# Kernel tuning notes

Measured on AMD Instinct MI355X. Metric: run time of the kernel, lower is better.

The kernel has to match this reference:

```python
import jax, jax.numpy as jnp
import numpy as np

EPS = 1e-12  # F.normalize default eps (denominator = max(norm, eps))


def setup_inputs() -> dict:
    key = jax.random.key(0)
    ks = jax.random.split(key, 8)
    B, FIN, H, W = 4, 256, 64, 64
    N_MEM, SQ = 64, 16           # sqrt_fin = fin**0.5
    POS_CH = 2                    # PosEncoding concatenates one coord channel per dim
    CIN = FIN + POS_CH
    QK = N_MEM * SQ               # 1024
    # PosEncoding buffer: normalized coordinate grid in [-1, 1], shape [2, H, W]
    ys = jnp.linspace(-1.0, 1.0, H, dtype=jnp.float32)
    xs = jnp.linspace(-1.0, 1.0, W, dtype=jnp.float32)
    gy, gx = jnp.meshgrid(ys, xs, indexing='ij')
    pos = jnp.stack([gy, gx], axis=0)
    s = 0.02
    return {
        'x':    jax.random.normal(ks[0], (B, FIN, H, W), jnp.float32),
        'pos':  pos,
        'wq':   jax.random.normal(ks[1], (QK, CIN), jnp.float32) * s,
        'bq':   jnp.zeros((QK,), jnp.float32),
        'wk':   jax.random.normal(ks[2], (QK, CIN), jnp.float32) * s,
        'bk':   jnp.zeros((QK,), jnp.float32),
        'v':    jax.random.normal(ks[3], (N_MEM, FIN), jnp.float32) * s,
        'wout': jax.random.normal(ks[4], (FIN, FIN), jnp.float32) * s,
        'bout': jnp.zeros((FIN,), jnp.float32),
    }


def reference(x, pos, wq, bq, wk, bk, v, wout, bout):
    B, C, H, W = x.shape
    S = H * W
    n_mem, fin = v.shape
    sq = wq.shape[0] // n_mem
    # PosEncoding: concat coordinate channels
    posb = jnp.broadcast_to(pos[None], (B,) + pos.shape)
    xp = jnp.concatenate([x, posb], axis=1).reshape(B, C + pos.shape[0], S)
    # 1x1 conv projections (channel GEMMs)
    q = jnp.einsum('oc,bcs->bos', wq, xp) + bq[None, :, None]  # [B, n_mem*sq, S]
    k = jnp.einsum('oc,bcs->bos', wk, xp) + bk[None, :, None]
    q = q.reshape(B, n_mem, sq, S).transpose(0, 3, 1, 2)  # [B,S,m,sq]
    k = k.reshape(B, n_mem, sq, S).transpose(0, 3, 2, 1)  # [B,S,sq,m]
    # F.normalize: q over last dim (sqrt_fin), k over dim=1 (sqrt_fin)
    qn = q / jnp.maximum(jnp.linalg.norm(q, axis=-1, keepdims=True), EPS)
    kn = k / jnp.maximum(jnp.linalg.norm(k, axis=2, keepdims=True), EPS)
    # attn[b,s,m,n] = qn . kn ; dropout is identity in eval mode.
    # mean over memory slots m commutes with (attn @ v), so fuse:
    attn_mean = jnp.einsum('bsk,bskn->bsn', qn.mean(axis=2), kn)  # [B,S,n_mem]
    mem = attn_mean @ v                                            # [B,S,fin]
    mem = mem.transpose(0, 2, 1).reshape(B, fin, H, W)
    out = jnp.einsum('of,bfhw->bohw', wout, mem) + bout[None, :, None, None]
    return x + out
```

## Files before the change

kernel.cpp:

```cpp
#include <hip/hip_runtime.h>
#include <stdint.h>

#define EPSN 1e-12f

typedef float f32x16 __attribute__((ext_vector_type(16)));
typedef float f32x4 __attribute__((ext_vector_type(4)));
typedef __bf16 bf16x8 __attribute__((ext_vector_type(8)));
typedef unsigned short u16x4 __attribute__((ext_vector_type(4)));

__device__ __forceinline__ unsigned short f2bf(float f) {
  union { float f; unsigned int u; } v; v.f = f;
  unsigned int u = v.u + 0x7FFFu + ((v.u >> 16) & 1u);
  return (unsigned short)(u >> 16);
}
__device__ __forceinline__ float bf2f(unsigned short h) {
  union { float f; unsigned int u; } v; v.u = ((unsigned int)h) << 16;
  return v.f;
}

#define NKS 17
#define WQF_OFF 0
#define WKF_OFF (32 * NKS * 64 * 8)
#define WVP_OFF (2 * 32 * NKS * 64 * 8)

__global__ __launch_bounds__(256) void prep_kernel(
    const float* __restrict__ wq, const float* __restrict__ bq,
    const float* __restrict__ wk, const float* __restrict__ bk,
    const float* __restrict__ v, const float* __restrict__ wout,
    unsigned short* __restrict__ wsp) {
  int bid = blockIdx.x;
  if (bid < 512) {
    int isK = bid >= 256;
    int ob = (bid & 255) * 4;
    const float* w = isK ? wk : wq;
    const float* bb = isK ? bk : bq;
    unsigned short* dst = wsp + (isK ? WKF_OFF : WQF_OFF);
    for (int i = threadIdx.x; i < 4 * 129; i += 256) {
      int r = i / 129, q = i - r * 129;
      int o = ob + r, k = q * 2;
      float2 w2 = *(const float2*)(w + o * 258 + k);
      int g = o >> 5, col = o & 31;
      int ks = k >> 4, hi = (k >> 3) & 1, j = k & 7;
      uint32_t pk = (uint32_t)f2bf(w2.x) | ((uint32_t)f2bf(w2.y) << 16);
      *(uint32_t*)(dst + (((g * NKS + ks) * 64 + hi * 32 + col) << 3) + j) = pk;
    }
    for (int i = threadIdx.x; i < 4 * 14; i += 256) {
      int r = i / 14, kk = 258 + (i - r * 14);
      int o = ob + r;
      int g = o >> 5, col = o & 31;
      int ks = kk >> 4, hi = (kk >> 3) & 1, j = kk & 7;
      dst[(((g * NKS + ks) * 64 + hi * 32 + col) << 3) + j] =
          (kk == 258) ? f2bf(bb[o]) : (unsigned short)0;
    }
  } else {
    int idx = (bid - 512) * 256 + threadIdx.x;
    int fc = idx & 15, m = (idx >> 4) & 63, o = idx >> 10;
    const f32x4* wo = (const f32x4*)(wout + o * 256 + fc * 16);
    const f32x4* vm = (const f32x4*)(v + m * 256 + fc * 16);
    float s = 0.f;
#pragma unroll
    for (int f = 0; f < 4; ++f) {
      f32x4 a = wo[f], bvv = vm[f];
      s += a[0]*bvv[0] + a[1]*bvv[1] + a[2]*bvv[2] + a[3]*bvv[3];
    }
    s += __shfl_xor(s, 1, 64);
    s += __shfl_xor(s, 2, 64);
    s += __shfl_xor(s, 4, 64);
    s += __shfl_xor(s, 8, 64);
    if (fc == 0) wsp[WVP_OFF + o * 64 + m] = f2bf(s);
  }
}

#define PXB 64
#define KP 296
#define QS 66
#define AT 72

__global__ __launch_bounds__(1024, 4) void fused_kernel(
    const float* __restrict__ x, const float* __restrict__ pos,
    const unsigned short* __restrict__ wsp, const float* __restrict__ bout,
    float* __restrict__ out) {
  __shared__ __align__(16) unsigned short xp[PXB * KP];
  __shared__ __align__(16) float qbarL[16 * QS];
  __shared__ __align__(16) unsigned short attnM[PXB * AT];
  __shared__ float boutL[256];

  const int tid = threadIdx.x;
  const int lane = tid & 63;
  const int wid = __builtin_amdgcn_readfirstlane(tid >> 6);
  const int px = lane & 31, q2 = lane >> 5;
  const int P0 = blockIdx.x * PXB;
  const int b = P0 >> 12, s0 = P0 & 4095;

  const int wtoff = (2 * wid) * NKS * 512 + lane * 8;
  const unsigned short* wqf = wsp + WQF_OFF + wtoff;
  const unsigned short* wkf = wsp + WKF_OFF + wtoff;

  uint32_t* xp32 = (uint32_t*)xp;
  {
    const float* xrow = x + b * 256 * 4096 + s0;
    f32x4 lo[2], hi[2];
#pragma unroll
    for (int it = 0; it < 2; ++it) {
      int idx = tid + it * 1024;
      int g = idx & 15, dcol = idx >> 4;
      lo[it] = __builtin_nontemporal_load(
          (const f32x4*)(xrow + (2 * dcol) * 4096 + 4 * g));
      hi[it] = __builtin_nontemporal_load(
          (const f32x4*)(xrow + (2 * dcol + 1) * 4096 + 4 * g));
    }
#pragma unroll
    for (int it = 0; it < 2; ++it) {
      int idx = tid + it * 1024;
      int g = idx & 15, dcol = idx >> 4;
#pragma unroll
      for (int j = 0; j < 4; ++j) {
        int pp = 4 * g + j;
        xp32[pp * 148 + dcol] =
            (uint32_t)f2bf(lo[it][j]) | ((uint32_t)f2bf(hi[it][j]) << 16);
      }
    }
    if (tid < 512) {
      int pp = tid & 63, dcol = 128 + (tid >> 6);
      float t0 = 0.f, t1 = 0.f;
      if (dcol == 128) { t0 = pos[s0 + pp]; t1 = pos[4096 + s0 + pp]; }
      else if (dcol == 129) { t0 = 1.0f; }
      xp32[pp * 148 + dcol] = (uint32_t)f2bf(t0) | ((uint32_t)f2bf(t1) << 16);
    }
  }
  if (tid < 256) boutL[tid] = bout[tid];
  for (int i = tid; i < 16 * QS; i += 1024) qbarL[i] = 0.f;
  __syncthreads();

#define PHASE(WB) do {                                                    \
    const unsigned short* _p0 = (WB);                                     \
    const unsigned short* _p1 = (WB) + NKS * 512;                         \
    const unsigned short* _bp0 = &xp[px * KP + q2 * 8];                   \
    const unsigned short* _bp1 = &xp[(32 + px) * KP + q2 * 8];            \
    bf16x8 _A0c = *(const bf16x8*)_p0;                                    \
    bf16x8 _A1c = *(const bf16x8*)_p1;                                    \
    _Pragma("unroll 1")                                                   \
    for (int i = 0; i < NKS - 1; ++i) {                                   \
      bf16x8 _A0n = *(const bf16x8*)(_p0 + (i + 1) * 512);                \
      bf16x8 _A1n = *(const bf16x8*)(_p1 + (i + 1) * 512);                \
      bf16x8 _b0 = *(const bf16x8*)(_bp0 + i * 16);                       \
      bf16x8 _b1 = *(const bf16x8*)(_bp1 + i * 16);                       \
      __builtin_amdgcn_s_setprio(1);                                      \
      acc00 = __builtin_amdgcn_mfma_f32_32x32x16_bf16(_A0c, _b0, acc00, 0, 0, 0); \
      acc01 = __builtin_amdgcn_mfma_f32_32x32x16_bf16(_A0c, _b1, acc01, 0, 0, 0); \
      acc10 = __builtin_amdgcn_mfma_f32_32x32x16_bf16(_A1c, _b0, acc10, 0, 0, 0); \
      acc11 = __builtin_amdgcn_mfma_f32_32x32x16_bf16(_A1c, _b1, acc11, 0, 0, 0); \
      __builtin_amdgcn_s_setprio(0);                                      \
      _A0c = _A0n; _A1c = _A1n;                                           \
    }                                                                     \
    {                                                                     \
      bf16x8 _b0 = *(const bf16x8*)(_bp0 + (NKS - 1) * 16);               \
      bf16x8 _b1 = *(const bf16x8*)(_bp1 + (NKS - 1) * 16);               \
      acc00 = __builtin_amdgcn_mfma_f32_32x32x16_bf16(_A0c, _b0, acc00, 0, 0, 0); \
      acc01 = __builtin_amdgcn_mfma_f32_32x32x16_bf16(_A0c, _b1, acc01, 0, 0, 0); \
      acc10 = __builtin_amdgcn_mfma_f32_32x32x16_bf16(_A1c, _b0, acc10, 0, 0, 0); \
      acc11 = __builtin_amdgcn_mfma_f32_32x32x16_bf16(_A1c, _b1, acc11, 0, 0, 0); \
    }                                                                     \
  } while (0)

  f32x16 acc00 = (f32x16)0.f, acc01 = (f32x16)0.f,
         acc10 = (f32x16)0.f, acc11 = (f32x16)0.f;
  PHASE(wqf);

  {
    float qsum[2][8];
#pragma unroll
    for (int nt = 0; nt < 2; ++nt)
#pragma unroll
      for (int r = 0; r < 8; ++r) qsum[nt][r] = 0.f;
#pragma unroll
    for (int ot = 0; ot < 2; ++ot) {
#pragma unroll
      for (int nt = 0; nt < 2; ++nt) {
        const f32x16 a = ot ? (nt ? acc11 : acc10) : (nt ? acc01 : acc00);
        float s20 = 0.f, s21 = 0.f;
#pragma unroll
        for (int r = 0; r < 8; ++r) {
          s20 = fmaf(a[r], a[r], s20);
          s21 = fmaf(a[r + 8], a[r + 8], s21);
        }
        s20 += __shfl_xor(s20, 32, 64);
        s21 += __shfl_xor(s21, 32, 64);
        float i0 = 1.0f / fmaxf(sqrtf(s20), EPSN);
        float i1 = 1.0f / fmaxf(sqrtf(s21), EPSN);
#pragma unroll
        for (int r = 0; r < 8; ++r) qsum[nt][r] += a[r] * i0 + a[r + 8] * i1;
      }
    }
#pragma unroll
    for (int nt = 0; nt < 2; ++nt)
#pragma unroll
      for (int r = 0; r < 8; ++r) {
        int j = (r & 3) + ((r >> 2) << 3) + (q2 << 2);
        atomicAdd(&qbarL[j * QS + nt * 32 + px], qsum[nt][r] * (1.0f / 64.0f));
      }
  }

  acc00 = (f32x16)0.f; acc01 = (f32x16)0.f;
  acc10 = (f32x16)0.f; acc11 = (f32x16)0.f;
  PHASE(wkf);
  __syncthreads();

  {
    float qb[2][8];
#pragma unroll
    for (int nt = 0; nt < 2; ++nt)
#pragma unroll
      for (int r = 0; r < 8; ++r) {
        int j = (r & 3) + ((r >> 2) << 3) + (q2 << 2);
        qb[nt][r] = qbarL[j * QS + nt * 32 + px];
      }
#pragma unroll
    for (int ot = 0; ot < 2; ++ot) {
#pragma unroll
      for (int nt = 0; nt < 2; ++nt) {
        const f32x16 a = ot ? (nt ? acc11 : acc10) : (nt ? acc01 : acc00);
        float s20 = 0.f, s21 = 0.f, sp0 = 0.f, sp1 = 0.f;
#pragma unroll
        for (int r = 0; r < 8; ++r) {
          s20 = fmaf(a[r], a[r], s20);         sp0 = fmaf(qb[nt][r], a[r], sp0);
          s21 = fmaf(a[r + 8], a[r + 8], s21); sp1 = fmaf(qb[nt][r], a[r + 8], sp1);
        }
        s20 += __shfl_xor(s20, 32, 64);
        s21 += __shfl_xor(s21, 32, 64);
        sp0 += __shfl_xor(sp0, 32, 64);
        sp1 += __shfl_xor(sp1, 32, 64);
        if (q2 == 0) {
          int m0 = wid * 4 + ot * 2;
          attnM[(nt * 32 + px) * AT + m0]     = f2bf(sp0 / fmaxf(sqrtf(s20), EPSN));
          attnM[(nt * 32 + px) * AT + m0 + 1] = f2bf(sp1 / fmaxf(sqrtf(s21), EPSN));
        }
      }
    }
  }
  __syncthreads();

  {
    const int otile = wid >> 1, pxt = wid & 1;
    f32x16 e = (f32x16)0.f;
    const unsigned short* wv = wsp + WVP_OFF + (otile * 32 + px) * 64 + q2 * 8;
    const unsigned short* ab = &attnM[(pxt * 32 + px) * AT + q2 * 8];
#pragma unroll
    for (int ks = 0; ks < 4; ++ks) {
      bf16x8 av = *(const bf16x8*)(wv + ks * 16);
      bf16x8 bv = *(const bf16x8*)(ab + ks * 16);
      e = __builtin_amdgcn_mfma_f32_32x32x16_bf16(av, bv, e, 0, 0, 0);
    }
    const int p = pxt * 32 + px;
    const unsigned short* xl = &xp[p * KP + otile * 32 + (q2 << 2)];
#pragma unroll
    for (int rq = 0; rq < 4; ++rq) {
      u16x4 xq = *(const u16x4*)(xl + 8 * rq);
#pragma unroll
      for (int j = 0; j < 4; ++j) {
        const int r = rq * 4 + j;
        const int o = otile * 32 + j + (rq << 3) + (q2 << 2);
        const int gi = (b * 256 + o) * 4096 + s0 + p;
        __builtin_nontemporal_store(bf2f(xq[j]) + boutL[o] + e[r], &out[gi]);
      }
    }
  }
#undef PHASE
}

extern "C" void kernel_launch(void* const* d_in, const int* in_sizes, int n_in,
                              void* d_out, int out_size, void* d_ws, size_t ws_size,
                              hipStream_t stream) {
  const float* x    = (const float*)d_in[0];
  const float* pos  = (const float*)d_in[1];
  const float* wq   = (const float*)d_in[2];
  const float* bq   = (const float*)d_in[3];
  const float* wk   = (const float*)d_in[4];
  const float* bk   = (const float*)d_in[5];
  const float* v    = (const float*)d_in[6];
  const float* wout = (const float*)d_in[7];
  const float* bout = (const float*)d_in[8];
  float* out = (float*)d_out;
  unsigned short* wsp = (unsigned short*)d_ws;

  hipLaunchKernelGGL(prep_kernel, dim3(1536), dim3(256), 0, stream,
                     wq, bq, wk, bk, v, wout, wsp);
  hipLaunchKernelGGL(fused_kernel, dim3(256), dim3(1024), 0, stream,
                     x, pos, wsp, bout, out);
}
```

Baseline: 127.8 us.

## Switch Q/K projection GEMMs from bf16 to fp8 MFMA and reload residual from global

Converts the Q and K projection weights and the staged input tile to fp8 (e4m3) and uses the fp8 32x32x16 MFMA in place of the bf16 one. This halves the weight and LDS traffic for the main GEMM phase. The residual add now rereads x from global memory in fp32 because the LDS tile is fp8 and too coarse. That adds a second read of x and lowers the precision of the attention logits, so accuracy tolerance becomes a risk.

```diff
diff --git a/kernel.cpp b/kernel.cpp
--- a/kernel.cpp
+++ b/kernel.cpp
@@ -6,51 +6,55 @@
 typedef float f32x16 __attribute__((ext_vector_type(16)));
 typedef float f32x4 __attribute__((ext_vector_type(4)));
 typedef __bf16 bf16x8 __attribute__((ext_vector_type(8)));
-typedef unsigned short u16x4 __attribute__((ext_vector_type(4)));
+typedef long long i64x2 __attribute__((ext_vector_type(2)));
 
 __device__ __forceinline__ unsigned short f2bf(float f) {
   union { float f; unsigned int u; } v; v.f = f;
   unsigned int u = v.u + 0x7FFFu + ((v.u >> 16) & 1u);
   return (unsigned short)(u >> 16);
 }
-__device__ __forceinline__ float bf2f(unsigned short h) {
-  union { float f; unsigned int u; } v; v.u = ((unsigned int)h) << 16;
-  return v.f;
+
+__device__ __forceinline__ unsigned short f2fp8x2(float a, float b) {
+  int r = __builtin_amdgcn_cvt_pk_fp8_f32(a, b, 0, false);
+  return (unsigned short)(r & 0xFFFF);
 }
 
 #define NKS 17
-#define WQF_OFF 0
-#define WKF_OFF (32 * NKS * 64 * 8)
-#define WVP_OFF (2 * 32 * NKS * 64 * 8)
+#define WQF_B 0
+#define WKF_B (16 * NKS * 64 * 16)
+#define WVP_OFF_S (2 * 16 * NKS * 64 * 8)
 
 __global__ __launch_bounds__(256) void prep_kernel(
     const float* __restrict__ wq, const float* __restrict__ bq,
     const float* __restrict__ wk, const float* __restrict__ bk,
     const float* __restrict__ v, const float* __restrict__ wout,
     unsigned short* __restrict__ wsp) {
+  uint8_t* wsp8 = (uint8_t*)wsp;
   int bid = blockIdx.x;
   if (bid < 512) {
     int isK = bid >= 256;
     int ob = (bid & 255) * 4;
     const float* w = isK ? wk : wq;
     const float* bb = isK ? bk : bq;
-    unsigned short* dst = wsp + (isK ? WKF_OFF : WQF_OFF);
+    uint8_t* dst = wsp8 + (isK ? WKF_B : WQF_B);
     for (int i = threadIdx.x; i < 4 * 129; i += 256) {
       int r = i / 129, q = i - r * 129;
       int o = ob + r, k = q * 2;
       float2 w2 = *(const float2*)(w + o * 258 + k);
-      int g = o >> 5, col = o & 31;
+      int g = o >> 5, col = o & 31, g2 = g >> 1, t = g & 1;
       int ks = k >> 4, hi = (k >> 3) & 1, j = k & 7;
-      uint32_t pk = (uint32_t)f2bf(w2.x) | ((uint32_t)f2bf(w2.y) << 16);
-      *(uint32_t*)(dst + (((g * NKS + ks) * 64 + hi * 32 + col) << 3) + j) = pk;
+      unsigned short pk = f2fp8x2(w2.x, w2.y);
+      *(unsigned short*)(dst +
+          (((g2 * NKS + ks) * 64 + hi * 32 + col) << 4) + t * 8 + j) = pk;
     }
     for (int i = threadIdx.x; i < 4 * 14; i += 256) {
       int r = i / 14, kk = 258 + (i - r * 14);
       int o = ob + r;
-      int g = o >> 5, col = o & 31;
+      int g = o >> 5, col = o & 31, g2 = g >> 1, t = g & 1;
       int ks = kk >> 4, hi = (kk >> 3) & 1, j = kk & 7;
-      dst[(((g * NKS + ks) * 64 + hi * 32 + col) << 3) + j] =
-          (kk == 258) ? f2bf(bb[o]) : (unsigned short)0;
+      uint8_t val = (kk == 258) ? (uint8_t)(f2fp8x2(bb[o], 0.f) & 0xFF)
+                                : (uint8_t)0;
+      dst[(((g2 * NKS + ks) * 64 + hi * 32 + col) << 4) + t * 8 + j] = val;
     }
   } else {
     int idx = (bid - 512) * 256 + threadIdx.x;
@@ -67,12 +71,12 @@
     s += __shfl_xor(s, 2, 64);
     s += __shfl_xor(s, 4, 64);
     s += __shfl_xor(s, 8, 64);
-    if (fc == 0) wsp[WVP_OFF + o * 64 + m] = f2bf(s);
+    if (fc == 0) wsp[WVP_OFF_S + o * 64 + m] = f2bf(s);
   }
 }
 
 #define PXB 64
-#define KP 296
+#define KP8 296
 #define QS 66
 #define AT 72
 
@@ -80,7 +84,7 @@
     const float* __restrict__ x, const float* __restrict__ pos,
     const unsigned short* __restrict__ wsp, const float* __restrict__ bout,
     float* __restrict__ out) {
-  __shared__ __align__(16) unsigned short xp[PXB * KP];
+  __shared__ __align__(16) uint8_t xp8[PXB * KP8];
   __shared__ __align__(16) float qbarL[16 * QS];
   __shared__ __align__(16) unsigned short attnM[PXB * AT];
   __shared__ float boutL[256];
@@ -92,11 +96,10 @@
   const int P0 = blockIdx.x * PXB;
   const int b = P0 >> 12, s0 = P0 & 4095;
 
-  const int wtoff = (2 * wid) * NKS * 512 + lane * 8;
-  const unsigned short* wqf = wsp + WQF_OFF + wtoff;
-  const unsigned short* wkf = wsp + WKF_OFF + wtoff;
-
-  uint32_t* xp32 = (uint32_t*)xp;
+  const uint8_t* wsp8 = (const uint8_t*)wsp;
+  const uint8_t* wqf = wsp8 + WQF_B + wid * (NKS * 1024) + lane * 16;
+  const uint8_t* wkf = wsp8 + WKF_B + wid * (NKS * 1024) + lane * 16;
+
   {
     const float* xrow = x + b * 256 * 4096 + s0;
     f32x4 lo[2], hi[2];
@@ -116,8 +119,8 @@
 #pragma unroll
       for (int j = 0; j < 4; ++j) {
         int pp = 4 * g + j;
-        xp32[pp * 148 + dcol] =
-            (uint32_t)f2bf(lo[it][j]) | ((uint32_t)f2bf(hi[it][j]) << 16);
+        *(unsigned short*)&xp8[pp * KP8 + 2 * dcol] =
+            f2fp8x2(lo[it][j], hi[it][j]);
       }
     }
     if (tid < 512) {
@@ -125,7 +128,7 @@
       float t0 = 0.f, t1 = 0.f;
       if (dcol == 128) { t0 = pos[s0 + pp]; t1 = pos[4096 + s0 + pp]; }
       else if (dcol == 129) { t0 = 1.0f; }
-      xp32[pp * 148 + dcol] = (uint32_t)f2bf(t0) | ((uint32_t)f2bf(t1) << 16);
+      *(unsigned short*)&xp8[pp * KP8 + 2 * dcol] = f2fp8x2(t0, t1);
     }
   }
   if (tid < 256) boutL[tid] = bout[tid];
@@ -133,33 +136,30 @@
   __syncthreads();
 
 #define PHASE(WB) do {                                                    \
-    const unsigned short* _p0 = (WB);                                     \
-    const unsigned short* _p1 = (WB) + NKS * 512;                         \
-    const unsigned short* _bp0 = &xp[px * KP + q2 * 8];                   \
-    const unsigned short* _bp1 = &xp[(32 + px) * KP + q2 * 8];            \
-    bf16x8 _A0c = *(const bf16x8*)_p0;                                    \
-    bf16x8 _A1c = *(const bf16x8*)_p1;                                    \
+    const uint8_t* _p = (WB);                                             \
+    const uint8_t* _b0p = &xp8[px * KP8 + q2 * 8];                        \
+    const uint8_t* _b1p = &xp8[(32 + px) * KP8 + q2 * 8];                 \
+    i64x2 _Ac = *(const i64x2*)_p;                                        \
     _Pragma("unroll 1")                                                   \
     for (int i = 0; i < NKS - 1; ++i) {                                   \
-      bf16x8 _A0n = *(const bf16x8*)(_p0 + (i + 1) * 512);                \
-      bf16x8 _A1n = *(const bf16x8*)(_p1 + (i + 1) * 512);                \
-      bf16x8 _b0 = *(const bf16x8*)(_bp0 + i * 16);                       \
-      bf16x8 _b1 = *(const bf16x8*)(_bp1 + i * 16);                       \
+      i64x2 _An = *(const i64x2*)(_p + (i + 1) * 1024);                   \
+      long long _b0 = *(const long long*)(_b0p + i * 16);                 \
+      long long _b1 = *(const long long*)(_b1p + i * 16);                 \
       __builtin_amdgcn_s_setprio(1);                                      \
-      acc00 = __builtin_amdgcn_mfma_f32_32x32x16_bf16(_A0c, _b0, acc00, 0, 0, 0); \
-      acc01 = __builtin_amdgcn_mfma_f32_32x32x16_bf16(_A0c, _b1, acc01, 0, 0, 0); \
-      acc10 = __builtin_amdgcn_mfma_f32_32x32x16_bf16(_A1c, _b0, acc10, 0, 0, 0); \
-      acc11 = __builtin_amdgcn_mfma_f32_32x32x16_bf16(_A1c, _b1, acc11, 0, 0, 0); \
+      acc00 = __builtin_amdgcn_mfma_f32_32x32x16_fp8_fp8(_Ac[0], _b0, acc00, 0, 0, 0); \
+      acc01 = __builtin_amdgcn_mfma_f32_32x32x16_fp8_fp8(_Ac[0], _b1, acc01, 0, 0, 0); \
+      acc10 = __builtin_amdgcn_mfma_f32_32x32x16_fp8_fp8(_Ac[1], _b0, acc10, 0, 0, 0); \
+      acc11 = __builtin_amdgcn_mfma_f32_32x32x16_fp8_fp8(_Ac[1], _b1, acc11, 0, 0, 0); \
       __builtin_amdgcn_s_setprio(0);                                      \
-      _A0c = _A0n; _A1c = _A1n;                                           \
+      _Ac = _An;                                                          \
     }                                                                     \
     {                                                                     \
-      bf16x8 _b0 = *(const bf16x8*)(_bp0 + (NKS - 1) * 16);               \
-      bf16x8 _b1 = *(const bf16x8*)(_bp1 + (NKS - 1) * 16);               \
-      acc00 = __builtin_amdgcn_mfma_f32_32x32x16_bf16(_A0c, _b0, acc00, 0, 0, 0); \
-      acc01 = __builtin_amdgcn_mfma_f32_32x32x16_bf16(_A0c, _b1, acc01, 0, 0, 0); \
-      acc10 = __builtin_amdgcn_mfma_f32_32x32x16_bf16(_A1c, _b0, acc10, 0, 0, 0); \
-      acc11 = __builtin_amdgcn_mfma_f32_32x32x16_bf16(_A1c, _b1, acc11, 0, 0, 0); \
+      long long _b0 = *(const long long*)(_b0p + (NKS - 1) * 16);         \
+      long long _b1 = *(const long long*)(_b1p + (NKS - 1) * 16);         \
+      acc00 = __builtin_amdgcn_mfma_f32_32x32x16_fp8_fp8(_Ac[0], _b0, acc00, 0, 0, 0); \
+      acc01 = __builtin_amdgcn_mfma_f32_32x32x16_fp8_fp8(_Ac[0], _b1, acc01, 0, 0, 0); \
+      acc10 = __builtin_amdgcn_mfma_f32_32x32x16_fp8_fp8(_Ac[1], _b0, acc10, 0, 0, 0); \
+      acc11 = __builtin_amdgcn_mfma_f32_32x32x16_fp8_fp8(_Ac[1], _b1, acc11, 0, 0, 0); \
     }                                                                     \
   } while (0)
 
@@ -243,7 +243,8 @@
   {
     const int otile = wid >> 1, pxt = wid & 1;
     f32x16 e = (f32x16)0.f;
-    const unsigned short* wv = wsp + WVP_OFF + (otile * 32 + px) * 64 + q2 * 8;
+    const unsigned short* wv =
+        wsp + WVP_OFF_S + (otile * 32 + px) * 64 + q2 * 8;
     const unsigned short* ab = &attnM[(pxt * 32 + px) * AT + q2 * 8];
 #pragma unroll
     for (int ks = 0; ks < 4; ++ks) {
@@ -252,17 +253,12 @@
       e = __builtin_amdgcn_mfma_f32_32x32x16_bf16(av, bv, e, 0, 0, 0);
     }
     const int p = pxt * 32 + px;
-    const unsigned short* xl = &xp[p * KP + otile * 32 + (q2 << 2)];
-#pragma unroll
-    for (int rq = 0; rq < 4; ++rq) {
-      u16x4 xq = *(const u16x4*)(xl + 8 * rq);
-#pragma unroll
-      for (int j = 0; j < 4; ++j) {
-        const int r = rq * 4 + j;
-        const int o = otile * 32 + j + (rq << 3) + (q2 << 2);
-        const int gi = (b * 256 + o) * 4096 + s0 + p;
-        __builtin_nontemporal_store(bf2f(xq[j]) + boutL[o] + e[r], &out[gi]);
-      }
+#pragma unroll
+    for (int r = 0; r < 16; ++r) {
+      const int o = otile * 32 + (r & 3) + ((r >> 2) << 3) + (q2 << 2);
+      const int gi = (b * 256 + o) * 4096 + s0 + p;
+      float xv = __builtin_nontemporal_load(&x[gi]);
+      __builtin_nontemporal_store(xv + boutL[o] + e[r], &out[gi]);
     }
   }
 #undef PHASE
```

Result: no change. 127.8 us (-0.0%).
